# Performance work log

Measured on AMD Instinct MI355X. Metric: run time of the kernel, lower is better.

The kernel has to match this reference:

```python
import jax, jax.numpy as jnp
import numpy as np

B, C, D, H, W = 8, 512, 512, 128, 128


def setup_inputs() -> dict:
    key = jax.random.key(0)
    ks = jax.random.split(key, 6)
    s = 0.02  # small init scale for stable softmax
    return {
        "x": jax.random.normal(ks[0], (B, C, H, W), dtype=jnp.float32),
        "context": jax.random.normal(ks[1], (B, D), dtype=jnp.float32),
        "Wq": jax.random.normal(ks[2], (C, D), dtype=jnp.float32) * s,
        "bq": jnp.ones((C,), dtype=jnp.float32),
        "Wk": jax.random.normal(ks[3], (C, C), dtype=jnp.float32) * s,
        "bk": jnp.zeros((C,), dtype=jnp.float32),
        "Wv": jax.random.normal(ks[4], (C, C), dtype=jnp.float32) * s,
        "bv": jnp.zeros((C,), dtype=jnp.float32),
    }


def reference(x, context, Wq, bq, Wk, bk, Wv, bv):
    # x: (B,C,H,W), context: (B,D)
    scale = x.shape[1] ** (-0.5)
    # q_proj: Linear(D -> C), single query per batch element
    q = context @ Wq.T + bq                      # (B, C)
    # 1x1 convs are channel-mixing GEMMs over the spatial grid
    k = jnp.einsum('bchw,oc->bohw', x, Wk) + bk[None, :, None, None]  # (B,C,H,W)
    v = jnp.einsum('bchw,oc->bohw', x, Wv) + bv[None, :, None, None]  # (B,C,H,W)
    # attention logits over the HW positions (query length == 1)
    logits = jnp.einsum('bc,bchw->bhw', q, k) * scale                 # (B,H,W)
    Bn, Hn, Wn = logits.shape
    attn = jax.nn.softmax(logits.reshape(Bn, Hn * Wn), axis=-1).reshape(Bn, Hn, Wn)
    # attention-pooled value -> channel gate
    gate = jnp.einsum('bhw,bchw->bc', attn, v)                        # (B,C)
    return x * gate[:, :, None, None]
```

## Files before the change

kernel.cpp:

```cpp
#include <hip/hip_runtime.h>
#include <math.h>

#define BB   8
#define CC   512
#define DD   512
#define HW   16384
#define HW4  4096
#define NCHUNK 64


__global__ __launch_bounds__(256) void k_qproj(const float* __restrict__ ctx,
                                               const float* __restrict__ Wq,
                                               const float* __restrict__ bq,
                                               float* __restrict__ q) {
    int t = blockIdx.x * 256 + threadIdx.x;
    int b = t >> 9, c = t & (CC - 1);
    const float4* cr = (const float4*)(ctx + (size_t)b * DD);
    const float4* wr = (const float4*)(Wq + (size_t)c * DD);
    float acc = 0.f;
    #pragma unroll 8
    for (int d = 0; d < DD / 4; ++d) {
        float4 a = cr[d], w = wr[d];
        acc += a.x * w.x + a.y * w.y + a.z * w.z + a.w * w.w;
    }
    q[t] = acc + bq[c];
}

__global__ __launch_bounds__(256) void k_qk(const float* __restrict__ q,
                                            const float* __restrict__ Wk,
                                            float* __restrict__ qk) {
    __shared__ float qs[CC];
    int b = blockIdx.x >> 1;
    int c = (blockIdx.x & 1) * 256 + threadIdx.x;
    for (int i = threadIdx.x; i < CC; i += 256) qs[i] = q[b * CC + i];
    __syncthreads();
    float acc = 0.f;
    #pragma unroll 8
    for (int o = 0; o < CC; ++o) acc += qs[o] * Wk[(size_t)o * CC + c];
    qk[b * CC + c] = acc;
}

__global__ __launch_bounds__(256) void k_fused(const float* __restrict__ x,
                                               const float* __restrict__ qk,
                                               float* __restrict__ part,
                                               float* __restrict__ stats) {
    __shared__ float  qs[CC];
    __shared__ float4 comb[3][64];
    __shared__ float4 p4s[64];
    __shared__ float  partLDS[CC];
    int b     = blockIdx.x >> 6;
    int chunk = blockIdx.x & 63;
    int wave = threadIdx.x >> 6, lane = threadIdx.x & 63;
    int hw4 = chunk * 64 + lane;
    for (int i = threadIdx.x; i < CC; i += 256) qs[i] = qk[b * CC + i];
    __syncthreads();
    const float4* x4 = (const float4*)x;
    size_t base = (size_t)b * CC * HW4 + (size_t)(wave * 128) * HW4 + hw4;
    float ax = 0.f, ay = 0.f, az = 0.f, aw = 0.f;
    #pragma unroll 8
    for (int c = 0; c < 128; ++c) {
        float4 v = x4[base + (size_t)c * HW4];
        float w = qs[wave * 128 + c];
        ax += w * v.x; ay += w * v.y; az += w * v.z; aw += w * v.w;
    }
    if (wave > 0) {
        float4 p = { ax, ay, az, aw };
        comb[wave - 1][lane] = p;
    }
    __syncthreads();
    if (wave == 0) {
        #pragma unroll
        for (int w2 = 0; w2 < 3; ++w2) {
            float4 p = comb[w2][lane];
            ax += p.x; ay += p.y; az += p.z; aw += p.w;
        }
        const float scale = 0.04419417382415922f;
        ax *= scale; ay *= scale; az *= scale; aw *= scale;
        float m = fmaxf(fmaxf(ax, ay), fmaxf(az, aw));
        #pragma unroll
        for (int off = 32; off; off >>= 1) m = fmaxf(m, __shfl_xor(m, off));
        float4 p;
        p.x = expf(ax - m); p.y = expf(ay - m);
        p.z = expf(az - m); p.w = expf(aw - m);
        float s = p.x + p.y + p.z + p.w;
        #pragma unroll
        for (int off = 32; off; off >>= 1) s += __shfl_xor(s, off);
        p4s[lane] = p;
        if (lane == 0) { stats[blockIdx.x * 2] = m; stats[blockIdx.x * 2 + 1] = s; }
    }
    __syncthreads();
    float4 pv = p4s[lane];
    #pragma unroll 4
    for (int c = 127; c >= 0; --c) {
        float4 v = x4[base + (size_t)c * HW4];
        float r = pv.x * v.x + pv.y * v.y + pv.z * v.z + pv.w * v.w;
        #pragma unroll
        for (int off = 32; off; off >>= 1) r += __shfl_down(r, off);
        if (lane == 0) partLDS[wave * 128 + c] = r;
    }
    __syncthreads();
    float4* pr = (float4*)(part + (size_t)blockIdx.x * CC);
    for (int i = threadIdx.x; i < CC / 4; i += 256) pr[i] = ((float4*)partLDS)[i];
}

__global__ __launch_bounds__(256) void k_combine(const float* __restrict__ part,
                                                 const float* __restrict__ stats,
                                                 float* __restrict__ pooled) {
    __shared__ float wgt[NCHUNK];
    int b = blockIdx.x, tid = threadIdx.x;
    if (tid < 64) {
        float mc = stats[(b * NCHUNK + tid) * 2];
        float sc = stats[(b * NCHUNK + tid) * 2 + 1];
        float m = mc;
        #pragma unroll
        for (int off = 32; off; off >>= 1) m = fmaxf(m, __shfl_xor(m, off));
        float w = expf(mc - m);
        float d = w * sc;
        #pragma unroll
        for (int off = 32; off; off >>= 1) d += __shfl_xor(d, off);
        wgt[tid] = w / d;
    }
    __syncthreads();
    for (int c = tid; c < CC; c += 256) {
        float acc = 0.f;
        #pragma unroll 8
        for (int ch = 0; ch < NCHUNK; ++ch)
            acc += wgt[ch] * part[(size_t)(b * NCHUNK + ch) * CC + c];
        pooled[b * CC + c] = acc;
    }
}

__global__ __launch_bounds__(256) void k_gate(const float* __restrict__ pooled,
                                              const float* __restrict__ Wv,
                                              const float* __restrict__ bv,
                                              float* __restrict__ gate) {
    int t = blockIdx.x * 256 + threadIdx.x;
    int b = t >> 9, o = t & (CC - 1);
    const float4* pr = (const float4*)(pooled + (size_t)b * CC);
    const float4* wr = (const float4*)(Wv + (size_t)o * CC);
    float acc = 0.f;
    #pragma unroll 8
    for (int i = 0; i < CC / 4; ++i) {
        float4 p = pr[i], w = wr[i];
        acc += p.x * w.x + p.y * w.y + p.z * w.z + p.w * w.w;
    }
    gate[t] = acc + bv[o];
}

__global__ __launch_bounds__(256) void k_out(const float* __restrict__ x,
                                             const float* __restrict__ gate,
                                             float* __restrict__ out) {
    int bc = blockIdx.x;
    float g = gate[bc];
    const float4* xr = (const float4*)x   + (size_t)bc * HW4;
    float4*       orow = (float4*)out     + (size_t)bc * HW4;
    #pragma unroll 8
    for (int i = threadIdx.x; i < HW4; i += 256) {
        float4 v = xr[i];
        float4 o = { v.x * g, v.y * g, v.z * g, v.w * g };
        orow[i] = o;
    }
}

extern "C" void kernel_launch(void* const* d_in, const int* in_sizes, int n_in,
                              void* d_out, int out_size, void* d_ws, size_t ws_size,
                              hipStream_t stream) {
    const float* x   = (const float*)d_in[0];
    const float* ctx = (const float*)d_in[1];
    const float* Wq  = (const float*)d_in[2];
    const float* bq  = (const float*)d_in[3];
    const float* Wk  = (const float*)d_in[4];
    const float* Wv  = (const float*)d_in[6];
    const float* bv  = (const float*)d_in[7];
    float* out = (float*)d_out;

    float* ws     = (float*)d_ws;
    float* q      = ws;
    float* qk     = ws + 4096;
    float* pooled = ws + 8192;
    float* gate   = ws + 12288;
    float* stats  = ws + 16384;
    float* part   = ws + 17408;

    k_qproj  <<<  16, 256, 0, stream>>>(ctx, Wq, bq, q);
    k_qk     <<<  16, 256, 0, stream>>>(q, Wk, qk);
    k_fused  <<< 512, 256, 0, stream>>>(x, qk, part, stats);
    k_combine<<<  BB, 256, 0, stream>>>(part, stats, pooled);
    k_gate   <<<  16, 256, 0, stream>>>(pooled, Wv, bv, gate);
    k_out    <<<4096, 256, 0, stream>>>(x, gate, out);
}
```

Baseline: 643.2 us.

## Split attention pooling into separate logits and per-channel pool kernels

The fused logits+pooling kernel is split: the first kernel writes unnormalized softmax weights to workspace, and a new 4096-block kernel computes each channel's pooled value as a streaming dot product over x and the weights. This removes the per-channel wave shuffle reductions and the partial-sum combine stage, and raises parallelism. The cost is a second full read of x from memory instead of relying on a cache-resident re-read. The q projection is also folded into the qk kernel to save a launch, at the cost of redundant q computation per block.

```diff
diff --git a/kernel.cpp b/kernel.cpp
--- a/kernel.cpp
+++ b/kernel.cpp
@@ -9,45 +9,39 @@
 #define NCHUNK 64
 
 
-__global__ __launch_bounds__(256) void k_qproj(const float* __restrict__ ctx,
-                                               const float* __restrict__ Wq,
-                                               const float* __restrict__ bq,
-                                               float* __restrict__ q) {
-    int t = blockIdx.x * 256 + threadIdx.x;
-    int b = t >> 9, c = t & (CC - 1);
+__global__ __launch_bounds__(256) void k_qk2(const float* __restrict__ ctx,
+                                             const float* __restrict__ Wq,
+                                             const float* __restrict__ bq,
+                                             const float* __restrict__ Wk,
+                                             float* __restrict__ qk) {
+    __shared__ float qs[CC];
+    int b    = blockIdx.x >> 1;
+    int half = blockIdx.x & 1;
     const float4* cr = (const float4*)(ctx + (size_t)b * DD);
-    const float4* wr = (const float4*)(Wq + (size_t)c * DD);
-    float acc = 0.f;
-    #pragma unroll 8
-    for (int d = 0; d < DD / 4; ++d) {
-        float4 a = cr[d], w = wr[d];
-        acc += a.x * w.x + a.y * w.y + a.z * w.z + a.w * w.w;
+    for (int c = threadIdx.x; c < CC; c += 256) {
+        const float4* wr = (const float4*)(Wq + (size_t)c * DD);
+        float acc = 0.f;
+        #pragma unroll 8
+        for (int d = 0; d < DD / 4; ++d) {
+            float4 a = cr[d], w = wr[d];
+            acc += a.x * w.x + a.y * w.y + a.z * w.z + a.w * w.w;
+        }
+        qs[c] = acc + bq[c];
     }
-    q[t] = acc + bq[c];
-}
-
-__global__ __launch_bounds__(256) void k_qk(const float* __restrict__ q,
-                                            const float* __restrict__ Wk,
-                                            float* __restrict__ qk) {
-    __shared__ float qs[CC];
-    int b = blockIdx.x >> 1;
-    int c = (blockIdx.x & 1) * 256 + threadIdx.x;
-    for (int i = threadIdx.x; i < CC; i += 256) qs[i] = q[b * CC + i];
     __syncthreads();
+    int c = half * 256 + threadIdx.x;
     float acc = 0.f;
     #pragma unroll 8
     for (int o = 0; o < CC; ++o) acc += qs[o] * Wk[(size_t)o * CC + c];
     qk[b * CC + c] = acc;
 }
 
-__global__ __launch_bounds__(256) void k_fused(const float* __restrict__ x,
-                                               const float* __restrict__ qk,
-                                               float* __restrict__ part,
-                                               float* __restrict__ stats) {
+__global__ __launch_bounds__(256) void k_logits_p(const float* __restrict__ x,
+                                                  const float* __restrict__ qk,
+                                                  float* __restrict__ p,
+                                                  float* __restrict__ stats) {
     __shared__ float  qs[CC];
     __shared__ float4 comb[3][64];
-    __shared__ float4 p4s[64];
-    __shared__ float  partLDS[CC];
     int b     = blockIdx.x >> 6;
     int chunk = blockIdx.x & 63;
     int wave = threadIdx.x >> 6, lane = threadIdx.x & 63;
@@ -64,50 +58,40 @@
         ax += w * v.x; ay += w * v.y; az += w * v.z; aw += w * v.w;
     }
     if (wave > 0) {
-        float4 p = { ax, ay, az, aw };
-        comb[wave - 1][lane] = p;
+        float4 pp = { ax, ay, az, aw };
+        comb[wave - 1][lane] = pp;
     }
     __syncthreads();
     if (wave == 0) {
         #pragma unroll
         for (int w2 = 0; w2 < 3; ++w2) {
-            float4 p = comb[w2][lane];
-            ax += p.x; ay += p.y; az += p.z; aw += p.w;
+            float4 pp = comb[w2][lane];
+            ax += pp.x; ay += pp.y; az += pp.z; aw += pp.w;
         }
         const float scale = 0.04419417382415922f;
         ax *= scale; ay *= scale; az *= scale; aw *= scale;
         float m = fmaxf(fmaxf(ax, ay), fmaxf(az, aw));
         #pragma unroll
         for (int off = 32; off; off >>= 1) m = fmaxf(m, __shfl_xor(m, off));
-        float4 p;
-        p.x = expf(ax - m); p.y = expf(ay - m);
-        p.z = expf(az - m); p.w = expf(aw - m);
-        float s = p.x + p.y + p.z + p.w;
+        float4 o;
+        o.x = expf(ax - m); o.y = expf(ay - m);
+        o.z = expf(az - m); o.w = expf(aw - m);
+        float s = o.x + o.y + o.z + o.w;
         #pragma unroll
         for (int off = 32; off; off >>= 1) s += __shfl_xor(s, off);
-        p4s[lane] = p;
+        ((float4*)p)[(size_t)b * HW4 + hw4] = o;
         if (lane == 0) { stats[blockIdx.x * 2] = m; stats[blockIdx.x * 2 + 1] = s; }
     }
-    __syncthreads();
-    float4 pv = p4s[lane];
-    #pragma unroll 4
-    for (int c = 127; c >= 0; --c) {
-        float4 v = x4[base + (size_t)c * HW4];
-        float r = pv.x * v.x + pv.y * v.y + pv.z * v.z + pv.w * v.w;
-        #pragma unroll
-        for (int off = 32; off; off >>= 1) r += __shfl_down(r, off);
-        if (lane == 0) partLDS[wave * 128 + c] = r;
-    }
-    __syncthreads();
-    float4* pr = (float4*)(part + (size_t)blockIdx.x * CC);
-    for (int i = threadIdx.x; i < CC / 4; i += 256) pr[i] = ((float4*)partLDS)[i];
 }
 
-__global__ __launch_bounds__(256) void k_combine(const float* __restrict__ part,
-                                                 const float* __restrict__ stats,
-                                                 float* __restrict__ pooled) {
+__global__ __launch_bounds__(256) void k_pool(const float* __restrict__ x,
+                                              const float* __restrict__ p,
+                                              const float* __restrict__ stats,
+                                              float* __restrict__ pooled) {
     __shared__ float wgt[NCHUNK];
-    int b = blockIdx.x, tid = threadIdx.x;
+    int bc = blockIdx.x;
+    int b  = bc >> 9;
+    int tid = threadIdx.x;
     if (tid < 64) {
         float mc = stats[(b * NCHUNK + tid) * 2];
         float sc = stats[(b * NCHUNK + tid) * 2 + 1];
@@ -121,13 +105,19 @@
         wgt[tid] = w / d;
     }
     __syncthreads();
-    for (int c = tid; c < CC; c += 256) {
-        float acc = 0.f;
-        #pragma unroll 8
-        for (int ch = 0; ch < NCHUNK; ++ch)
-            acc += wgt[ch] * part[(size_t)(b * NCHUNK + ch) * CC + c];
-        pooled[b * CC + c] = acc;
+    const float4* xr = (const float4*)x + (size_t)bc * HW4;
+    const float4* pr = (const float4*)p + (size_t)b  * HW4;
+    float acc = 0.f;
+    #pragma unroll 8
+    for (int i = tid; i < HW4; i += 256) {
+        float4 xv = xr[i], pv = pr[i];
+        acc += wgt[i >> 6] * (xv.x * pv.x + xv.y * pv.y + xv.z * pv.z + xv.w * pv.w);
     }
+    for (int off = 32; off; off >>= 1) acc += __shfl_down(acc, off);
+    __shared__ float red[4];
+    if ((tid & 63) == 0) red[tid >> 6] = acc;
+    __syncthreads();
+    if (tid == 0) pooled[bc] = red[0] + red[1] + red[2] + red[3];
 }
 
 __global__ __launch_bounds__(256) void k_gate(const float* __restrict__ pooled,
@@ -141,8 +131,8 @@
     float acc = 0.f;
     #pragma unroll 8
     for (int i = 0; i < CC / 4; ++i) {
-        float4 p = pr[i], w = wr[i];
-        acc += p.x * w.x + p.y * w.y + p.z * w.z + p.w * w.w;
+        float4 pv = pr[i], w = wr[i];
+        acc += pv.x * w.x + pv.y * w.y + pv.z * w.z + pv.w * w.w;
     }
     gate[t] = acc + bv[o];
 }
@@ -175,17 +165,15 @@
     float* out = (float*)d_out;
 
     float* ws     = (float*)d_ws;
-    float* q      = ws;
-    float* qk     = ws + 4096;
-    float* pooled = ws + 8192;
-    float* gate   = ws + 12288;
-    float* stats  = ws + 16384;
-    float* part   = ws + 17408;
+    float* qk     = ws;
+    float* pooled = ws + 4096;
+    float* gate   = ws + 8192;
+    float* stats  = ws + 12288;
+    float* p      = ws + 13312;
 
-    k_qproj  <<<  16, 256, 0, stream>>>(ctx, Wq, bq, q);
-    k_qk     <<<  16, 256, 0, stream>>>(q, Wk, qk);
-    k_fused  <<< 512, 256, 0, stream>>>(x, qk, part, stats);
-    k_combine<<<  BB, 256, 0, stream>>>(part, stats, pooled);
-    k_gate   <<<  16, 256, 0, stream>>>(pooled, Wv, bv, gate);
-    k_out    <<<4096, 256, 0, stream>>>(x, gate, out);
+    k_qk2     <<<  16, 256, 0, stream>>>(ctx, Wq, bq, Wk, qk);
+    k_logits_p<<< 512, 256, 0, stream>>>(x, qk, p, stats);
+    k_pool    <<<4096, 256, 0, stream>>>(x, p, stats, pooled);
+    k_gate    <<<  16, 256, 0, stream>>>(pooled, Wv, bv, gate);
+    k_out     <<<4096, 256, 0, stream>>>(x, gate, out);
 }
```

After: 618.9 us. -3.8%, faster.
